# Kernel optimization log

Measured on AMD Instinct MI355X. Metric: run time of the kernel, lower is better.

## Reference

```python
import jax, jax.numpy as jnp
import numpy as np

N = 100000   # total atoms in batch of graphs
E = 400000   # directed edges
B = 1024     # graphs / proteins in batch
F_XD = 78    # atom feature dim
DIM = 32     # GIN hidden dim
OUT_DIM = 128
EMB = 128    # protein token embed dim
VOCAB = 26   # num_features_xt + 1
NF = 32      # conv1d filters
SEQ = 1000
K = 8        # conv1d kernel size
LM = 1024    # LM embedding dim
FLAT = NF * (SEQ - K + 1)  # 31776
COMB = 2 * OUT_DIM + 2 * LM  # 2304


def setup_inputs() -> dict:
    key = jax.random.key(0)
    ks = jax.random.split(key, 40)
    s = 0.05  # weight scale
    nrm = lambda k, shape: (jax.random.normal(k, shape, jnp.float32) * s)
    inp = {
        'x': jax.random.normal(ks[0], (N, F_XD), jnp.float32),
        'edge_index': jax.random.randint(ks[1], (2, E), 0, N),
        'batch': jnp.sort(jax.random.randint(ks[2], (N,), 0, B)),
        'target': jax.random.randint(ks[3], (B, SEQ), 0, VOCAB),
        'drug_lm': jax.random.normal(ks[4], (B, LM), jnp.float32),
        'protein_lm': jax.random.normal(ks[5], (B, LM), jnp.float32),
        # GINConv 1 MLP (78->32->32)
        'w1a': nrm(ks[6], (F_XD, DIM)), 'b1a': jnp.zeros((DIM,), jnp.float32),
        'w1b': nrm(ks[7], (DIM, DIM)), 'b1b': jnp.zeros((DIM,), jnp.float32),
        # GINConv 2-5 MLPs stacked (32->32->32)
        'gw_a': nrm(ks[8], (4, DIM, DIM)), 'gb_a': jnp.zeros((4, DIM), jnp.float32),
        'gw_b': nrm(ks[9], (4, DIM, DIM)), 'gb_b': jnp.zeros((4, DIM), jnp.float32),
        # BatchNorm affine params for 5 layers
        'bn_gamma': jnp.ones((5, DIM), jnp.float32),
        'bn_beta': jnp.zeros((5, DIM), jnp.float32),
        'fc1_xd_w': nrm(ks[10], (DIM, OUT_DIM)), 'fc1_xd_b': jnp.zeros((OUT_DIM,), jnp.float32),
        'emb': nrm(ks[11], (VOCAB, EMB)),
        'convxt_w': nrm(ks[12], (NF, EMB, K)), 'convxt_b': jnp.zeros((NF,), jnp.float32),
        'fc1_xt_w': nrm(ks[13], (FLAT, OUT_DIM)) * 0.1, 'fc1_xt_b': jnp.zeros((OUT_DIM,), jnp.float32),
        'fc1_w': nrm(ks[14], (COMB, 1024)), 'fc1_b': jnp.zeros((1024,), jnp.float32),
        'fc2_w': nrm(ks[15], (1024, 256)), 'fc2_b': jnp.zeros((256,), jnp.float32),
        'out_w': nrm(ks[16], (256, 1)), 'out_b': jnp.zeros((1,), jnp.float32),
    }
    return inp


def reference(x, edge_index, batch, target, drug_lm, protein_lm,
              w1a, b1a, w1b, b1b, gw_a, gb_a, gw_b, gb_b,
              bn_gamma, bn_beta, fc1_xd_w, fc1_xd_b, emb,
              convxt_w, convxt_b, fc1_xt_w, fc1_xt_b,
              fc1_w, fc1_b, fc2_w, fc2_b, out_w, out_b):
    src, dst = edge_index[0], edge_index[1]

    def bn(z, g, be):
        mu = z.mean(axis=0)
        var = jnp.mean((z - mu) ** 2, axis=0)
        return g * (z - mu) * jax.lax.rsqrt(var + 1e-5) + be

    def gin(h, wa, ba, wb, bb, g, be):
        # GIN aggregation: out_i = MLP((1+eps)*x_i + sum_{j->i} x_j), eps=0
        agg = jax.ops.segment_sum(h[src], dst, num_segments=N)
        z = jnp.maximum((h + agg) @ wa + ba, 0.0) @ wb + bb
        return bn(jnp.maximum(z, 0.0), g, be)  # relu then BatchNorm

    h = gin(x, w1a, b1a, w1b, b1b, bn_gamma[0], bn_beta[0])
    for i in range(4):  # convs 2..5
        h = gin(h, gw_a[i], gb_a[i], gw_b[i], gb_b[i], bn_gamma[i + 1], bn_beta[i + 1])

    xg = jax.ops.segment_sum(h, batch, num_segments=B)  # global_add_pool -> [B, 32]
    xg = jnp.maximum(xg @ fc1_xd_w + fc1_xd_b, 0.0)      # [B, 128]

    e = emb[target]                      # [B, SEQ, EMB]
    e = jnp.transpose(e, (0, 2, 1))      # [B, EMB, SEQ]
    c = jax.lax.conv_general_dilated(e, convxt_w, (1,), 'VALID',
                                     dimension_numbers=('NCH', 'OIH', 'NCH'))
    c = jnp.maximum(c + convxt_b[None, :, None], 0.0)    # [B, 32, 993]
    xt = jnp.maximum(c.reshape(B, -1) @ fc1_xt_w + fc1_xt_b, 0.0)  # [B, 128]

    xc = jnp.concatenate([xg, xt, drug_lm, protein_lm], axis=1)  # [B, 2304]
    xc = jnp.maximum(xc @ fc1_w + fc1_b, 0.0)
    xc = jnp.maximum(xc @ fc2_w + fc2_b, 0.0)
    return xc @ out_w + out_b  # [B, 1]
```

## Files before the change

kernel.cpp:

```cpp
#include <hip/hip_runtime.h>
#include <hip/hip_bf16.h>

#define NN 100000
#define EE 400000
#define BB 1024
#define FXD 78
#define DIMC 32
#define VOCABN 26
#define SEQN 1000
#define PCONV 993
#define FLATN 31776
#define COMB 2304
#define NB_SC 391

static __device__ __forceinline__ float relu_(float x) { return x > 0.f ? x : 0.f; }

template<int KC, bool TRANSFORM>
__global__ __launch_bounds__(256) void gin_gemm1(
    const float* __restrict__ H, const float* __restrict__ W, float* __restrict__ P,
    const float* __restrict__ sums, const float* __restrict__ gamma, const float* __restrict__ beta)
{
    __shared__ float As[32][KC + 1];
    __shared__ float Ws[KC][32];
    __shared__ float scale_s[32], shift_s[32];
    const int tid = threadIdx.x;
    const int row0 = blockIdx.x * 32;
    if (TRANSFORM) {
        if (tid < 32) {
            float mu = sums[tid] * (1.f / NN);
            float var = sums[32 + tid] * (1.f / NN) - mu * mu;
            float rs = rsqrtf(var + 1e-5f);
            float a = gamma[tid] * rs;
            scale_s[tid] = a;
            shift_s[tid] = beta[tid] - mu * a;
        }
    }
    for (int idx = tid; idx < KC * 32; idx += 256) Ws[idx / 32][idx % 32] = W[idx];
    __syncthreads();
    for (int idx = tid; idx < 32 * KC; idx += 256) {
        int r = idx / KC, k = idx % KC;
        float v = H[(row0 + r) * KC + k];
        if (TRANSFORM) v = v * scale_s[k] + shift_s[k];
        As[r][k] = v;
    }
    __syncthreads();
    const int col = tid & 31, rg = tid >> 5;
    float acc[4] = {0.f, 0.f, 0.f, 0.f};
    for (int k = 0; k < KC; ++k) {
        float w = Ws[k][col];
#pragma unroll
        for (int r = 0; r < 4; ++r) acc[r] += As[rg + 8 * r][k] * w;
    }
#pragma unroll
    for (int r = 0; r < 4; ++r) P[(row0 + rg + 8 * r) * 32 + col] = acc[r];
}

__global__ __launch_bounds__(256) void gin_gemm2(
    const float* __restrict__ P, const float* __restrict__ AGG, const float* __restrict__ W,
    const float* __restrict__ ba, const float* __restrict__ bb,
    float* __restrict__ Y, float* __restrict__ partials)
{
    __shared__ float As[32][33];
    __shared__ float Ws[32][32];
    __shared__ float red[8][32], red2[8][32];
    const int tid = threadIdx.x;
    const int row0 = blockIdx.x * 32;
    for (int idx = tid; idx < 1024; idx += 256) Ws[idx / 32][idx % 32] = W[idx];
    for (int idx = tid; idx < 1024; idx += 256) {
        int r = idx / 32, k = idx % 32;
        int g = (row0 + r) * 32 + k;
        As[r][k] = relu_(P[g] + AGG[g] + ba[k]);
    }
    __syncthreads();
    const int col = tid & 31, rg = tid >> 5;
    float acc[4] = {0.f, 0.f, 0.f, 0.f};
    for (int k = 0; k < 32; ++k) {
        float w = Ws[k][col];
#pragma unroll
        for (int r = 0; r < 4; ++r) acc[r] += As[rg + 8 * r][k] * w;
    }
    float s = 0.f, ss = 0.f;
#pragma unroll
    for (int r = 0; r < 4; ++r) {
        float y = relu_(acc[r] + bb[col]);
        Y[(row0 + rg + 8 * r) * 32 + col] = y;
        s += y; ss += y * y;
    }
    red[rg][col] = s; red2[rg][col] = ss;
    __syncthreads();
    if (tid < 32) {
        float t1 = 0.f, t2 = 0.f;
#pragma unroll
        for (int i = 0; i < 8; ++i) { t1 += red[i][tid]; t2 += red2[i][tid]; }
        partials[blockIdx.x * 64 + tid] = t1;
        partials[blockIdx.x * 64 + 32 + tid] = t2;
    }
}

__global__ __launch_bounds__(256) void hist_kernel(const int* __restrict__ dst, int* __restrict__ deg)
{
    int e = blockIdx.x * 256 + threadIdx.x;
    if (e < EE) atomicAdd(&deg[dst[e]], 1);
}

__global__ __launch_bounds__(256) void scan1_kernel(
    const int* __restrict__ deg, int* __restrict__ scanex, int* __restrict__ bsums)
{
    __shared__ int tmp[2][256];
    int tid = threadIdx.x, g = blockIdx.x * 256 + tid;
    int v = (g < NN) ? deg[g] : 0;
    tmp[0][tid] = v;
    __syncthreads();
    int cur = 0;
    for (int off = 1; off < 256; off <<= 1) {
        int nxt = cur ^ 1;
        tmp[nxt][tid] = tmp[cur][tid] + ((tid >= off) ? tmp[cur][tid - off] : 0);
        cur = nxt;
        __syncthreads();
    }
    int incl = tmp[cur][tid];
    if (g < NN) scanex[g] = incl - v;
    if (tid == 255) bsums[blockIdx.x] = incl;
}

__global__ __launch_bounds__(512) void scan2_kernel(const int* __restrict__ bsums, int* __restrict__ bexcl)
{
    __shared__ int tmp[2][512];
    int tid = threadIdx.x;
    int v = (tid < NB_SC) ? bsums[tid] : 0;
    tmp[0][tid] = v;
    __syncthreads();
    int cur = 0;
    for (int off = 1; off < 512; off <<= 1) {
        int nxt = cur ^ 1;
        tmp[nxt][tid] = tmp[cur][tid] + ((tid >= off) ? tmp[cur][tid - off] : 0);
        cur = nxt;
        __syncthreads();
    }
    if (tid < NB_SC) bexcl[tid] = tmp[cur][tid] - v;
}

__global__ __launch_bounds__(256) void rowptr_kernel(
    const int* __restrict__ scanex, const int* __restrict__ bexcl, int* __restrict__ rowptr)
{
    int g = blockIdx.x * 256 + threadIdx.x;
    if (g < NN) rowptr[g] = scanex[g] + bexcl[g >> 8];
    if (g == 0) rowptr[NN] = EE;
}

__global__ __launch_bounds__(256) void fill_kernel(
    const int* __restrict__ src, const int* __restrict__ dst,
    const int* __restrict__ rowptr, int* __restrict__ cursor, int* __restrict__ eidx)
{
    int e = blockIdx.x * 256 + threadIdx.x;
    if (e >= EE) return;
    int d = dst[e];
    int slot = rowptr[d] + atomicAdd(&cursor[d], 1);
    eidx[slot] = src[e];
}

__global__ __launch_bounds__(256) void gather_kernel(
    const int* __restrict__ rowptr, const int* __restrict__ eidx,
    const float* __restrict__ P, float* __restrict__ AGG)
{
    int t = blockIdx.x * 256 + threadIdx.x;
    int n = t >> 3, q = t & 7;
    if (n >= NN) return;
    int s = rowptr[n], e = rowptr[n + 1];
    float4 acc = make_float4(0.f, 0.f, 0.f, 0.f);
    for (int p = s; p < e; ++p) {
        int sn = eidx[p];
        float4 v = *(const float4*)&P[(size_t)sn * 32 + q * 4];
        acc.x += v.x; acc.y += v.y; acc.z += v.z; acc.w += v.w;
    }
    *(float4*)&AGG[(size_t)n * 32 + q * 4] = acc;
}

__global__ __launch_bounds__(256) void stat_reduce(const float* __restrict__ partials, float* __restrict__ sums)
{
    const int j = blockIdx.x;
    float s = 0.f;
    for (int i = threadIdx.x; i < 3125; i += 256) s += partials[i * 64 + j];
#pragma unroll
    for (int off = 32; off > 0; off >>= 1) s += __shfl_down(s, off);
    __shared__ float wsum[4];
    int w = threadIdx.x >> 6, lane = threadIdx.x & 63;
    if (lane == 0) wsum[w] = s;
    __syncthreads();
    if (threadIdx.x == 0) sums[j] = wsum[0] + wsum[1] + wsum[2] + wsum[3];
}

__global__ __launch_bounds__(256) void pool_kernel(
    const float* __restrict__ Y, const int* __restrict__ batch,
    const float* __restrict__ sums, const float* __restrict__ gamma, const float* __restrict__ beta,
    float* __restrict__ XG)
{
    __shared__ float scale_s[32], shift_s[32];
    int tid = threadIdx.x;
    if (tid < 32) {
        float mu = sums[tid] * (1.f / NN);
        float var = sums[32 + tid] * (1.f / NN) - mu * mu;
        float rs = rsqrtf(var + 1e-5f);
        float a = gamma[tid] * rs;
        scale_s[tid] = a; shift_s[tid] = beta[tid] - mu * a;
    }
    __syncthreads();
    int idx = blockIdx.x * 256 + tid;
    if (idx >= NN * 32) return;
    int i = idx >> 5, c = idx & 31;
    float v = Y[idx] * scale_s[c] + shift_s[c];
    atomicAdd(&XG[batch[i] * 32 + c], v);
}

__global__ __launch_bounds__(128) void fc_xd_kernel(
    const float* __restrict__ XG, const float* __restrict__ W, const float* __restrict__ b,
    float* __restrict__ XD)
{
    __shared__ float xs[32];
    int tid = threadIdx.x, blk = blockIdx.x;
    if (tid < 32) xs[tid] = XG[blk * 32 + tid];
    __syncthreads();
    float acc = b[tid];
    for (int k = 0; k < 32; ++k) acc += xs[k] * W[k * 128 + tid];
    XD[blk * 128 + tid] = relu_(acc);
}

__global__ __launch_bounds__(256) void mtable_kernel(
    const float* __restrict__ emb, const float* __restrict__ cw, float* __restrict__ M)
{
    int v = blockIdx.x, tid = threadIdx.x;
    int k = tid >> 5, f = tid & 31;
    float acc = 0.f;
    for (int c = 0; c < 128; ++c) acc += emb[v * 128 + c] * cw[f * 1024 + c * 8 + k];
    M[v * 256 + k * 32 + f] = acc;
}

__global__ __launch_bounds__(256) void conv_kernel(
    const int* __restrict__ target, const float* __restrict__ M, const float* __restrict__ cb,
    float* __restrict__ C)
{
    __shared__ float Ms[26 * 265];
    __shared__ int toks[136];
    int tid = threadIdx.x;
    int b = blockIdx.y, p0 = blockIdx.x * 128;
    for (int idx = tid; idx < 6656; idx += 256) {
        int v = idx >> 8, rem = idx & 255, k = rem >> 5, f = rem & 31;
        Ms[v * 265 + k * 33 + f] = M[idx];
    }
    for (int t = tid; t < 135; t += 256) {
        int p = p0 + t;
        toks[t] = (p < SEQN) ? target[b * SEQN + p] : 0;
    }
    __syncthreads();
    int pl = tid & 31, sub = tid >> 5;
    for (int it = 0; it < 16; ++it) {
        int chunk = it * 8 + sub;
        int f = chunk >> 2, pb = chunk & 3;
        int p = p0 + pb * 32 + pl;
        if (p < PCONV) {
            float acc = cb[f];
            int psub = pb * 32 + pl;
#pragma unroll
            for (int k = 0; k < 8; ++k) {
                int tok = toks[psub + k];
                acc += Ms[tok * 265 + k * 33 + f];
            }
            C[(size_t)b * FLATN + f * PCONV + p] = relu_(acc);
        }
    }
}

template<int TN>
__global__ __launch_bounds__(256) void gemm_v3(
    const float* __restrict__ A, const float* __restrict__ W,
    float* __restrict__ out, int lda, int ldw, int ldo, int k_end, int k_chunk)
{
    constexpr int NG = TN / 4;
    constexpr int MR = NG / 4;
    __shared__ float As[32][64 + 4];
    __shared__ float Ws[32][TN + 4];
    const int tid = threadIdx.x;
    const int m0 = blockIdx.x * 64, n0 = blockIdx.y * TN;
    const int kb = blockIdx.z * k_chunk;
    const int ke = min(kb + k_chunk, k_end);
    const int tx = tid % NG, ty = tid / NG;

    float4 acc[MR];
#pragma unroll
    for (int i = 0; i < MR; ++i) acc[i] = make_float4(0.f, 0.f, 0.f, 0.f);

    const int nk = (ke - kb) >> 5;
    for (int kit = 0; kit < nk; ++kit) {
        const int k0 = kb + kit * 32;
#pragma unroll
        for (int t = 0; t < 2; ++t) {
            int f4i = tid + t * 256;
            int r = f4i >> 3, c = f4i & 7;
            float4 v = *(const float4*)&A[(size_t)(m0 + r) * lda + k0 + 4 * c];
            As[4 * c + 0][r] = v.x; As[4 * c + 1][r] = v.y;
            As[4 * c + 2][r] = v.z; As[4 * c + 3][r] = v.w;
        }
#pragma unroll
        for (int t = 0; t < NG / 8; ++t) {
            int f4i = tid + t * 256;
            int kk = f4i / NG, n4 = f4i % NG;
            *(float4*)&Ws[kk][4 * n4] = *(const float4*)&W[(size_t)(k0 + kk) * ldw + n0 + 4 * n4];
        }
        __syncthreads();
#pragma unroll
        for (int kk = 0; kk < 32; ++kk) {
            float4 wv = *(const float4*)&Ws[kk][4 * tx];
#pragma unroll
            for (int j = 0; j < MR / 4; ++j) {
                float4 av = *(const float4*)&As[kk][MR * ty + 4 * j];
                float ar[4] = {av.x, av.y, av.z, av.w};
#pragma unroll
                for (int i = 0; i < 4; ++i) {
                    acc[4 * j + i].x += ar[i] * wv.x;
                    acc[4 * j + i].y += ar[i] * wv.y;
                    acc[4 * j + i].z += ar[i] * wv.z;
                    acc[4 * j + i].w += ar[i] * wv.w;
                }
            }
        }
        __syncthreads();
    }
    for (int k = kb + nk * 32; k < ke; ++k) {
        float4 wv = *(const float4*)&W[(size_t)k * ldw + n0 + 4 * tx];
#pragma unroll
        for (int i = 0; i < MR; ++i) {
            float a = A[(size_t)(m0 + MR * ty + i) * lda + k];
            acc[i].x += a * wv.x; acc[i].y += a * wv.y;
            acc[i].z += a * wv.z; acc[i].w += a * wv.w;
        }
    }

    float* dst = out + (size_t)blockIdx.z * (size_t)(gridDim.x * 64) * (size_t)ldo;
#pragma unroll
    for (int i = 0; i < MR; ++i)
        *(float4*)&dst[(size_t)(m0 + MR * ty + i) * ldo + n0 + 4 * tx] = acc[i];
}

__global__ __launch_bounds__(256) void splitk_reduce(
    const float* __restrict__ part, const float* __restrict__ bias,
    float* __restrict__ out, int MN, int N, int nz)
{
    int i4 = blockIdx.x * 256 + threadIdx.x;
    size_t base = (size_t)i4 * 4;
    if (base >= (size_t)MN) return;
    float4 s = make_float4(0.f, 0.f, 0.f, 0.f);
    for (int z = 0; z < nz; ++z) {
        float4 p = *(const float4*)&part[(size_t)z * MN + base];
        s.x += p.x; s.y += p.y; s.z += p.z; s.w += p.w;
    }
    int n0 = (int)(base % (size_t)N);
    float4 b = *(const float4*)&bias[n0];
    s.x = relu_(s.x + b.x); s.y = relu_(s.y + b.y);
    s.z = relu_(s.z + b.z); s.w = relu_(s.w + b.w);
    *(float4*)&out[base] = s;
}

__global__ __launch_bounds__(256) void concat_kernel(
    const float* __restrict__ XD, const float* __restrict__ XT,
    const float* __restrict__ drug, const float* __restrict__ prot, float* __restrict__ XC)
{
    int idx = blockIdx.x * 256 + threadIdx.x;
    if (idx >= BB * COMB) return;
    int b = idx / COMB, j = idx - b * COMB;
    float v;
    if (j < 128) v = XD[b * 128 + j];
    else if (j < 256) v = XT[b * 128 + (j - 128)];
    else if (j < 1280) v = drug[b * 1024 + (j - 256)];
    else v = prot[b * 1024 + (j - 1280)];
    XC[idx] = v;
}

__global__ __launch_bounds__(256) void out_kernel(
    const float* __restrict__ X, const float* __restrict__ ow, const float* __restrict__ ob,
    float* __restrict__ out)
{
    int wv = threadIdx.x >> 6, lane = threadIdx.x & 63;
    int b = blockIdx.x * 4 + wv;
    float acc = 0.f;
#pragma unroll
    for (int t = 0; t < 4; ++t) {
        int j = lane + t * 64;
        acc += X[b * 256 + j] * ow[j];
    }
#pragma unroll
    for (int off = 32; off > 0; off >>= 1) acc += __shfl_down(acc, off);
    if (lane == 0) out[b] = acc + ob[0];
}

extern "C" void kernel_launch(void* const* d_in, const int* in_sizes, int n_in,
                              void* d_out, int out_size, void* d_ws, size_t ws_size,
                              hipStream_t stream)
{
    (void)in_sizes; (void)n_in; (void)out_size; (void)ws_size;
    const float* x          = (const float*)d_in[0];
    const int*   edge       = (const int*)d_in[1];
    const int*   batch      = (const int*)d_in[2];
    const int*   target     = (const int*)d_in[3];
    const float* drug_lm    = (const float*)d_in[4];
    const float* protein_lm = (const float*)d_in[5];
    const float* w1a        = (const float*)d_in[6];
    const float* b1a        = (const float*)d_in[7];
    const float* w1b        = (const float*)d_in[8];
    const float* b1b        = (const float*)d_in[9];
    const float* gw_a       = (const float*)d_in[10];
    const float* gb_a       = (const float*)d_in[11];
    const float* gw_b       = (const float*)d_in[12];
    const float* gb_b       = (const float*)d_in[13];
    const float* bn_gamma   = (const float*)d_in[14];
    const float* bn_beta    = (const float*)d_in[15];
    const float* fc1_xd_w   = (const float*)d_in[16];
    const float* fc1_xd_b   = (const float*)d_in[17];
    const float* emb        = (const float*)d_in[18];
    const float* convxt_w   = (const float*)d_in[19];
    const float* convxt_b   = (const float*)d_in[20];
    const float* fc1_xt_w   = (const float*)d_in[21];
    const float* fc1_xt_b   = (const float*)d_in[22];
    const float* fc1_w      = (const float*)d_in[23];
    const float* fc1_b      = (const float*)d_in[24];
    const float* fc2_w      = (const float*)d_in[25];
    const float* fc2_b      = (const float*)d_in[26];
    const float* out_w      = (const float*)d_in[27];
    const float* out_b      = (const float*)d_in[28];
    float* out = (float*)d_out;

    char* ws = (char*)d_ws;
    size_t off = 0;
    auto alloc = [&](size_t bytes) -> void* {
        void* p = ws + off;
        off = (off + bytes + 255) & ~(size_t)255;
        return p;
    };
    float* P        = (float*)alloc((size_t)NN * 32 * 4);
    float* AGG      = (float*)alloc((size_t)NN * 32 * 4);
    float* Y0       = (float*)alloc((size_t)NN * 32 * 4);
    float* Y1       = (float*)alloc((size_t)NN * 32 * 4);
    float* partials = (float*)alloc((size_t)3125 * 64 * 4);
    float* sums     = (float*)alloc(64 * 4);
    float* XG       = (float*)alloc((size_t)BB * 32 * 4);
    float* XD       = (float*)alloc((size_t)BB * 128 * 4);
    float* Mt       = (float*)alloc((size_t)26 * 256 * 4);
    float* XT       = (float*)alloc((size_t)BB * 128 * 4);
    float* XC       = (float*)alloc((size_t)BB * COMB * 4);
    float* XC2      = (float*)alloc((size_t)BB * 1024 * 4);
    float* XC3      = (float*)alloc((size_t)BB * 256 * 4);
    float* C        = (float*)alloc((size_t)BB * FLATN * 4);

    float* xt_part  = P;
    float* fc1_part = C;
    float* fc2_part = C + (size_t)4 * 1024 * 1024;
    char*  csr      = (char*)C + (size_t)48 * 1024 * 1024;
    int* deg    = (int*)csr;
    int* cursor = deg + NN;
    int* scanex = cursor + NN;
    int* bsums  = scanex + NN;
    int* bexcl  = bsums + 512;
    int* rowptr = bexcl + 512;
    int* eidx   = rowptr + (NN + 2);

    const int* src = edge;
    const int* dst = edge + EE;

    mtable_kernel<<<26, 256, 0, stream>>>(emb, convxt_w, Mt);
    conv_kernel<<<dim3(8, BB), 256, 0, stream>>>(target, Mt, convxt_b, C);
    gemm_v3<128><<<dim3(16, 1, 32), 256, 0, stream>>>(
        C, fc1_xt_w, xt_part, FLATN, 128, 128, FLATN, PCONV);
    splitk_reduce<<<128, 256, 0, stream>>>(xt_part, fc1_xt_b, XT, BB * 128, 128, 32);

    hipMemsetAsync(deg, 0, (size_t)2 * NN * 4, stream);
    hist_kernel<<<1563, 256, 0, stream>>>(dst, deg);
    scan1_kernel<<<NB_SC, 256, 0, stream>>>(deg, scanex, bsums);
    scan2_kernel<<<1, 512, 0, stream>>>(bsums, bexcl);
    rowptr_kernel<<<NB_SC, 256, 0, stream>>>(scanex, bexcl, rowptr);
    fill_kernel<<<1563, 256, 0, stream>>>(src, dst, rowptr, cursor, eidx);

    gin_gemm1<78, false><<<3125, 256, 0, stream>>>(x, w1a, P, nullptr, nullptr, nullptr);
    gather_kernel<<<3125, 256, 0, stream>>>(rowptr, eidx, P, AGG);
    gin_gemm2<<<3125, 256, 0, stream>>>(P, AGG, w1b, b1a, b1b, Y0, partials);
    stat_reduce<<<64, 256, 0, stream>>>(partials, sums);

    float* yin = Y0; float* yout = Y1;
    for (int li = 0; li < 4; ++li) {
        gin_gemm1<32, true><<<3125, 256, 0, stream>>>(
            yin, gw_a + li * 1024, P, sums, bn_gamma + li * 32, bn_beta + li * 32);
        gather_kernel<<<3125, 256, 0, stream>>>(rowptr, eidx, P, AGG);
        gin_gemm2<<<3125, 256, 0, stream>>>(
            P, AGG, gw_b + li * 1024, gb_a + li * 32, gb_b + li * 32, yout, partials);
        stat_reduce<<<64, 256, 0, stream>>>(partials, sums);
        float* t = yin; yin = yout; yout = t;
    }

    hipMemsetAsync(XG, 0, (size_t)BB * 32 * 4, stream);
    pool_kernel<<<12500, 256, 0, stream>>>(yin, batch, sums, bn_gamma + 4 * 32, bn_beta + 4 * 32, XG);
    fc_xd_kernel<<<BB, 128, 0, stream>>>(XG, fc1_xd_w, fc1_xd_b, XD);

    concat_kernel<<<9216, 256, 0, stream>>>(XD, XT, drug_lm, protein_lm, XC);
    gemm_v3<128><<<dim3(16, 8, 4), 256, 0, stream>>>(
        XC, fc1_w, fc1_part, COMB, 1024, 1024, COMB, 576);
    splitk_reduce<<<1024, 256, 0, stream>>>(fc1_part, fc1_b, XC2, BB * 1024, 1024, 4);
    gemm_v3<128><<<dim3(16, 2, 8), 256, 0, stream>>>(
        XC2, fc2_w, fc2_part, 1024, 256, 256, 1024, 128);
    splitk_reduce<<<256, 256, 0, stream>>>(fc2_part, fc2_b, XC3, BB * 256, 256, 8);
    out_kernel<<<256, 256, 0, stream>>>(XC3, out_w, out_b, out);
}
```

Baseline: 787.2 us.

## Fuse protein conv1d into fc1_xt split-K GEMM, drop conv output buffer

The separate conv kernel wrote a 1024x31776 fp32 activation (about 130 MB) that the split-K GEMM then read back. Now the GEMM's A tile is computed on the fly from the token ids and a per-filter lookup table (emb times conv weight). Each of the 32 z-blocks handles one filter over all 993 positions, and the lookup table is re-laid out per filter. This removes the large intermediate write and read, at the cost of redundant token loads and LDS lookups inside the GEMM loop.

```diff
diff --git a/kernel.cpp b/kernel.cpp
--- a/kernel.cpp
+++ b/kernel.cpp
@@ -232,42 +232,87 @@
     int k = tid >> 5, f = tid & 31;
     float acc = 0.f;
     for (int c = 0; c < 128; ++c) acc += emb[v * 128 + c] * cw[f * 1024 + c * 8 + k];
-    M[v * 256 + k * 32 + f] = acc;
-}
-
-__global__ __launch_bounds__(256) void conv_kernel(
+    M[f * 208 + v * 8 + k] = acc;
+}
+
+__global__ __launch_bounds__(256) void xt_fused(
     const int* __restrict__ target, const float* __restrict__ M, const float* __restrict__ cb,
-    float* __restrict__ C)
-{
-    __shared__ float Ms[26 * 265];
-    __shared__ int toks[136];
-    int tid = threadIdx.x;
-    int b = blockIdx.y, p0 = blockIdx.x * 128;
-    for (int idx = tid; idx < 6656; idx += 256) {
-        int v = idx >> 8, rem = idx & 255, k = rem >> 5, f = rem & 31;
-        Ms[v * 265 + k * 33 + f] = M[idx];
-    }
-    for (int t = tid; t < 135; t += 256) {
-        int p = p0 + t;
-        toks[t] = (p < SEQN) ? target[b * SEQN + p] : 0;
-    }
-    __syncthreads();
-    int pl = tid & 31, sub = tid >> 5;
-    for (int it = 0; it < 16; ++it) {
-        int chunk = it * 8 + sub;
-        int f = chunk >> 2, pb = chunk & 3;
-        int p = p0 + pb * 32 + pl;
-        if (p < PCONV) {
-            float acc = cb[f];
-            int psub = pb * 32 + pl;
-#pragma unroll
-            for (int k = 0; k < 8; ++k) {
-                int tok = toks[psub + k];
-                acc += Ms[tok * 265 + k * 33 + f];
+    const float* __restrict__ W, float* __restrict__ out)
+{
+    __shared__ float As[32][68];
+    __shared__ float Ws[32][132];
+    __shared__ int   toks[64][41];
+    __shared__ float Ms[26 * 9];
+    const int tid = threadIdx.x;
+    const int m0 = blockIdx.x * 64;
+    const int f  = blockIdx.z;
+    const int tx = tid & 31, ty = tid >> 5;
+    const float cbf = cb[f];
+
+    for (int i = tid; i < 208; i += 256) Ms[(i >> 3) * 9 + (i & 7)] = M[f * 208 + i];
+    __syncthreads();
+
+    float4 acc[8];
+#pragma unroll
+    for (int i = 0; i < 8; ++i) acc[i] = make_float4(0.f, 0.f, 0.f, 0.f);
+
+    for (int p0 = 0; p0 < PCONV; p0 += 32) {
+#pragma unroll
+        for (int t = 0; t < 10; ++t) {
+            int idx = tid + t * 256;
+            int r = idx / 40, c = idx - r * 40;
+            int p = p0 + c;
+            toks[r][c] = (p < SEQN) ? target[(size_t)(m0 + r) * SEQN + p] : 0;
+        }
+#pragma unroll
+        for (int t = 0; t < 4; ++t) {
+            int f4i = tid + t * 256;
+            int kk = f4i >> 5, n4 = f4i & 31;
+            float4 wv = make_float4(0.f, 0.f, 0.f, 0.f);
+            if (p0 + kk < PCONV)
+                wv = *(const float4*)&W[(size_t)(f * PCONV + p0 + kk) * 128 + 4 * n4];
+            *(float4*)&Ws[kk][4 * n4] = wv;
+        }
+        __syncthreads();
+#pragma unroll
+        for (int t = 0; t < 8; ++t) {
+            int idx = tid + t * 256;
+            int r = idx & 63, kk = idx >> 6;
+            int p = p0 + kk;
+            float s = 0.f;
+            if (p < PCONV) {
+                s = cbf;
+#pragma unroll
+                for (int j = 0; j < 8; ++j)
+                    s += Ms[toks[r][kk + j] * 9 + j];
+                s = relu_(s);
             }
-            C[(size_t)b * FLATN + f * PCONV + p] = relu_(acc);
-        }
-    }
+            As[kk][r] = s;
+        }
+        __syncthreads();
+#pragma unroll
+        for (int kk = 0; kk < 32; ++kk) {
+            float4 wv = *(const float4*)&Ws[kk][4 * tx];
+#pragma unroll
+            for (int j = 0; j < 2; ++j) {
+                float4 av = *(const float4*)&As[kk][8 * ty + 4 * j];
+                float ar[4] = {av.x, av.y, av.z, av.w};
+#pragma unroll
+                for (int i = 0; i < 4; ++i) {
+                    acc[4 * j + i].x += ar[i] * wv.x;
+                    acc[4 * j + i].y += ar[i] * wv.y;
+                    acc[4 * j + i].z += ar[i] * wv.z;
+                    acc[4 * j + i].w += ar[i] * wv.w;
+                }
+            }
+        }
+        __syncthreads();
+    }
+
+    float* dst = out + (size_t)f * (size_t)(16 * 64) * 128;
+#pragma unroll
+    for (int i = 0; i < 8; ++i)
+        *(float4*)&dst[(size_t)(m0 + 8 * ty + i) * 128 + 4 * tx] = acc[i];
 }
 
 template<int TN>
@@ -448,12 +493,12 @@
     float* XC       = (float*)alloc((size_t)BB * COMB * 4);
     float* XC2      = (float*)alloc((size_t)BB * 1024 * 4);
     float* XC3      = (float*)alloc((size_t)BB * 256 * 4);
-    float* C        = (float*)alloc((size_t)BB * FLATN * 4);
+    float* SCR      = (float*)alloc((size_t)80 * 1024 * 1024);
 
     float* xt_part  = P;
-    float* fc1_part = C;
-    float* fc2_part = C + (size_t)4 * 1024 * 1024;
-    char*  csr      = (char*)C + (size_t)48 * 1024 * 1024;
+    float* fc1_part = SCR;
+    float* fc2_part = SCR + (size_t)4 * 1024 * 1024;
+    char*  csr      = (char*)SCR + (size_t)48 * 1024 * 1024;
     int* deg    = (int*)csr;
     int* cursor = deg + NN;
     int* scanex = cursor + NN;
@@ -466,9 +511,7 @@
     const int* dst = edge + EE;
 
     mtable_kernel<<<26, 256, 0, stream>>>(emb, convxt_w, Mt);
-    conv_kernel<<<dim3(8, BB), 256, 0, stream>>>(target, Mt, convxt_b, C);
-    gemm_v3<128><<<dim3(16, 1, 32), 256, 0, stream>>>(
-        C, fc1_xt_w, xt_part, FLATN, 128, 128, FLATN, PCONV);
+    xt_fused<<<dim3(16, 1, 32), 256, 0, stream>>>(target, Mt, convxt_b, fc1_xt_w, xt_part);
     splitk_reduce<<<128, 256, 0, stream>>>(xt_part, fc1_xt_b, XT, BB * 128, 128, 32);
 
     hipMemsetAsync(deg, 0, (size_t)2 * NN * 4, stream);
```

After: 865.3 us. 9.9% more time.

## Fuse CSR neighbor gather into GIN second GEMM and widen fc1_xt split-K

Applied to the files above, without the earlier changes.

Merges the neighbor aggregation gather into the second GIN MLP kernel, so the self term plus neighbor sum is computed directly into shared memory. This removes the AGG buffer write/read round-trip and one launch per layer. Separately, the fc1_xt GEMM split-K goes from 32 to 63 slices of 512 for more parallelism, at the cost of larger partial buffers. Those partials now spill past P into adjacent allocations, relying on allocation layout and ordering.

```diff
diff --git a/kernel.cpp b/kernel.cpp
--- a/kernel.cpp
+++ b/kernel.cpp
@@ -55,8 +55,9 @@
     for (int r = 0; r < 4; ++r) P[(row0 + rg + 8 * r) * 32 + col] = acc[r];
 }
 
-__global__ __launch_bounds__(256) void gin_gemm2(
-    const float* __restrict__ P, const float* __restrict__ AGG, const float* __restrict__ W,
+__global__ __launch_bounds__(256) void gin_gather_gemm2(
+    const int* __restrict__ rowptr, const int* __restrict__ eidx,
+    const float* __restrict__ P, const float* __restrict__ W,
     const float* __restrict__ ba, const float* __restrict__ bb,
     float* __restrict__ Y, float* __restrict__ partials)
 {
@@ -66,10 +67,21 @@
     const int tid = threadIdx.x;
     const int row0 = blockIdx.x * 32;
     for (int idx = tid; idx < 1024; idx += 256) Ws[idx / 32][idx % 32] = W[idx];
-    for (int idx = tid; idx < 1024; idx += 256) {
-        int r = idx / 32, k = idx % 32;
-        int g = (row0 + r) * 32 + k;
-        As[r][k] = relu_(P[g] + AGG[g] + ba[k]);
+    {
+        int r = tid >> 3, q = tid & 7;
+        int n = row0 + r;
+        int s = rowptr[n], e = rowptr[n + 1];
+        float4 acc = *(const float4*)&P[(size_t)n * 32 + q * 4];
+        for (int p = s; p < e; ++p) {
+            int sn = eidx[p];
+            float4 v = *(const float4*)&P[(size_t)sn * 32 + q * 4];
+            acc.x += v.x; acc.y += v.y; acc.z += v.z; acc.w += v.w;
+        }
+        float4 bv = *(const float4*)&ba[q * 4];
+        As[r][4 * q + 0] = relu_(acc.x + bv.x);
+        As[r][4 * q + 1] = relu_(acc.y + bv.y);
+        As[r][4 * q + 2] = relu_(acc.z + bv.z);
+        As[r][4 * q + 3] = relu_(acc.w + bv.w);
     }
     __syncthreads();
     const int col = tid & 31, rg = tid >> 5;
@@ -157,23 +169,6 @@
     int d = dst[e];
     int slot = rowptr[d] + atomicAdd(&cursor[d], 1);
     eidx[slot] = src[e];
-}
-
-__global__ __launch_bounds__(256) void gather_kernel(
-    const int* __restrict__ rowptr, const int* __restrict__ eidx,
-    const float* __restrict__ P, float* __restrict__ AGG)
-{
-    int t = blockIdx.x * 256 + threadIdx.x;
-    int n = t >> 3, q = t & 7;
-    if (n >= NN) return;
-    int s = rowptr[n], e = rowptr[n + 1];
-    float4 acc = make_float4(0.f, 0.f, 0.f, 0.f);
-    for (int p = s; p < e; ++p) {
-        int sn = eidx[p];
-        float4 v = *(const float4*)&P[(size_t)sn * 32 + q * 4];
-        acc.x += v.x; acc.y += v.y; acc.z += v.z; acc.w += v.w;
-    }
-    *(float4*)&AGG[(size_t)n * 32 + q * 4] = acc;
 }
 
 __global__ __launch_bounds__(256) void stat_reduce(const float* __restrict__ partials, float* __restrict__ sums)
@@ -452,7 +447,7 @@
 
     float* xt_part  = P;
     float* fc1_part = C;
-    float* fc2_part = C + (size_t)4 * 1024 * 1024;
+    float* fc2_part = C + (size_t)17 * 1024 * 1024 / 4;
     char*  csr      = (char*)C + (size_t)48 * 1024 * 1024;
     int* deg    = (int*)csr;
     int* cursor = deg + NN;
@@ -467,9 +462,9 @@
 
     mtable_kernel<<<26, 256, 0, stream>>>(emb, convxt_w, Mt);
     conv_kernel<<<dim3(8, BB), 256, 0, stream>>>(target, Mt, convxt_b, C);
-    gemm_v3<128><<<dim3(16, 1, 32), 256, 0, stream>>>(
-        C, fc1_xt_w, xt_part, FLATN, 128, 128, FLATN, PCONV);
-    splitk_reduce<<<128, 256, 0, stream>>>(xt_part, fc1_xt_b, XT, BB * 128, 128, 32);
+    gemm_v3<128><<<dim3(16, 1, 63), 256, 0, stream>>>(
+        C, fc1_xt_w, xt_part, FLATN, 128, 128, FLATN, 512);
+    splitk_reduce<<<128, 256, 0, stream>>>(xt_part, fc1_xt_b, XT, BB * 128, 128, 63);
 
     hipMemsetAsync(deg, 0, (size_t)2 * NN * 4, stream);
     hist_kernel<<<1563, 256, 0, stream>>>(dst, deg);
@@ -479,17 +474,15 @@
     fill_kernel<<<1563, 256, 0, stream>>>(src, dst, rowptr, cursor, eidx);
 
     gin_gemm1<78, false><<<3125, 256, 0, stream>>>(x, w1a, P, nullptr, nullptr, nullptr);
-    gather_kernel<<<3125, 256, 0, stream>>>(rowptr, eidx, P, AGG);
-    gin_gemm2<<<3125, 256, 0, stream>>>(P, AGG, w1b, b1a, b1b, Y0, partials);
+    gin_gather_gemm2<<<3125, 256, 0, stream>>>(rowptr, eidx, P, w1b, b1a, b1b, Y0, partials);
     stat_reduce<<<64, 256, 0, stream>>>(partials, sums);
 
     float* yin = Y0; float* yout = Y1;
     for (int li = 0; li < 4; ++li) {
         gin_gemm1<32, true><<<3125, 256, 0, stream>>>(
             yin, gw_a + li * 1024, P, sums, bn_gamma + li * 32, bn_beta + li * 32);
-        gather_kernel<<<3125, 256, 0, stream>>>(rowptr, eidx, P, AGG);
-        gin_gemm2<<<3125, 256, 0, stream>>>(
-            P, AGG, gw_b + li * 1024, gb_a + li * 32, gb_b + li * 32, yout, partials);
+        gin_gather_gemm2<<<3125, 256, 0, stream>>>(
+            rowptr, eidx, P, gw_b + li * 1024, gb_a + li * 32, gb_b + li * 32, yout, partials);
         stat_reduce<<<64, 256, 0, stream>>>(partials, sums);
         float* t = yin; yin = yout; yout = t;
     }
```

After: 777.4 us. Within noise of the previous version (-1.3%).
